# Optimization experiments

Measured on AMD Instinct MI355X. Metric: run time of the kernel, lower is better.

Reference implementation:

```python
import jax, jax.numpy as jnp
import numpy as np


def _vieta_pell_basis(x, degree):
    # Iterative recurrence: V0 = 2, V1 = x, Vn = x*V_{n-1} + V_{n-2}
    basis = [2.0 * jnp.ones_like(x), x]
    for _ in range(2, degree + 1):
        basis.append(x * basis[-1] + basis[-2])
    return jnp.stack(basis[: degree + 1], axis=-1)  # [b, i, d+1]


def setup_inputs() -> dict:
    key = jax.random.key(0)
    k1, k2 = jax.random.split(key)
    batch, input_dim, output_dim, degree = 4096, 1024, 1024, 8
    x = jax.random.normal(k1, (batch, input_dim), dtype=jnp.float32)
    std = 1.0 / (input_dim * (degree + 1))
    vp_coeffs = jax.random.normal(k2, (input_dim, output_dim, degree + 1), dtype=jnp.float32) * std
    return {"x": x, "vp_coeffs": vp_coeffs}


def reference(x, vp_coeffs):
    degree = vp_coeffs.shape[-1] - 1
    xt = jnp.tanh(x)  # [b, i]
    vp_basis = _vieta_pell_basis(xt, degree)  # [b, i, d+1]
    y = jnp.einsum("bid,iod->bo", vp_basis, vp_coeffs)
    return y
```

## Files before the change

kernel.cpp:

```cpp
#include <hip/hip_runtime.h>
#include <hip/hip_bf16.h>

typedef unsigned short u16;
typedef unsigned int   u32;
typedef unsigned long long u64;

#define BATCH 4096
#define IDIM  1024
#define ODIM  1024
#define NDEG  9
#define KTOT  (IDIM * NDEG)

#define BM 128
#define BN 128
#define BKK 64

typedef __attribute__((ext_vector_type(8))) short short8_t;
typedef __attribute__((ext_vector_type(4))) float f32x4;

__device__ __forceinline__ u16 f2bf(float f) {
    union { float f; u32 u; } v; v.f = f;
    u32 r = v.u + 0x7FFFu + ((v.u >> 16) & 1u);
    return (u16)(r >> 16);
}
__device__ __forceinline__ u32 pack2bf(float lo, float hi) {
    return (u32)f2bf(lo) | ((u32)f2bf(hi) << 16);
}

__device__ __forceinline__ void gl_lds16(const u16* g, u16* l) {
    __builtin_amdgcn_global_load_lds(
        (const __attribute__((address_space(1))) void*)g,
        (__attribute__((address_space(3))) void*)l,
        16, 0, 0);
}

#define PB_TI 128
#define PB_TO 8
#define PB_J  (PB_TO * NDEG)
#define PB_LS 132

#define NB_B   1024
#define NB_A   8192
#define NB_Z   256

__global__ void prep_kernel(const float* __restrict__ x,
                            const float* __restrict__ c,
                            u16* __restrict__ A, u16* __restrict__ Bt,
                            float* __restrict__ out) {
    __shared__ u16 lds[PB_J * PB_LS];
    const int bb  = blockIdx.x;
    const int tid = threadIdx.x;

    if (bb < NB_B) {
        const int i0 = (bb & 7) * PB_TI;
        const int o0 = (bb >> 3) * PB_TO;
        const float* src = c + (size_t)i0 * (ODIM * NDEG) + (size_t)o0 * NDEG;
#pragma unroll
        for (int t = 0; t < 36; ++t) {
            int f  = t * 256 + tid;
            int ii = f / PB_J;
            int j  = f - ii * PB_J;
            float v = src[(size_t)ii * (ODIM * NDEG) + j];
            lds[j * PB_LS + ii] = f2bf(v);
        }
        __syncthreads();
#pragma unroll
        for (int t = 0; t < 9; ++t) {
            int g   = t * 256 + tid;
            int j   = g >> 5;
            int ii4 = (g & 31) << 2;
            int o   = j / NDEG;
            int d   = j - o * NDEG;
            u64 v = *(const u64*)(lds + j * PB_LS + ii4);
            *(u64*)(Bt + (size_t)(o0 + o) * KTOT + d * 1024 + i0 + ii4) = v;
        }
    } else if (bb < NB_B + NB_A) {
        int t  = (bb - NB_B) * 256 + tid;
        int b  = t >> 9;
        int i2 = (t & 511) << 1;
        float2 xv = ((const float2*)x)[t];
        float t0 = tanhf(xv.x), t1 = tanhf(xv.y);
        u32* dst = (u32*)(A + (size_t)b * KTOT + i2);
        float a0 = 2.0f, a1 = 2.0f;
        float b0 = t0,  b1 = t1;
        dst[0]   = pack2bf(2.0f, 2.0f);
        dst[512] = pack2bf(t0, t1);
#pragma unroll
        for (int d = 2; d < NDEG; ++d) {
            float n0 = t0 * b0 + a0;
            float n1 = t1 * b1 + a1;
            dst[(size_t)d * 512] = pack2bf(n0, n1);
            a0 = b0; b0 = n0; a1 = b1; b1 = n1;
        }
    } else {
        int t = (bb - NB_B - NB_A) * 256 + tid;
        f32x4 z = (f32x4){0.f, 0.f, 0.f, 0.f};
#pragma unroll
        for (int r = 0; r < 16; ++r)
            ((f32x4*)out)[(size_t)r * (NB_Z * 256) + t] = z;
    }
}

__global__ __launch_bounds__(256, 2)
void gemm_kernel(const u16* __restrict__ A, const u16* __restrict__ B,
                 float* __restrict__ C, int kLen) {
    __shared__ __align__(16) u16 ldsA[BM * BKK];
    __shared__ __align__(16) u16 ldsB[BN * BKK];

    const int tid  = threadIdx.x;
    const int lane = tid & 63;
    const int wave = tid >> 6;
    const int quad = lane >> 4;
    const int l15  = lane & 15;
    const int wm   = wave & 1;
    const int wn   = wave >> 1;
    const int bm   = blockIdx.y;
    const int bn   = blockIdx.x;
    const int kStart = blockIdx.z * kLen;

    const u16* ga[4]; const u16* gb[4];
    u16* la[4]; u16* lb[4];
#pragma unroll
    for (int t = 0; t < 4; ++t) {
        int s  = t * 256 + tid;
        int r  = s >> 3;
        int sc = (s & 7) ^ (r & 7);
        ga[t] = A + (size_t)(bm * BM + r) * KTOT + kStart + sc * 8;
        gb[t] = B + (size_t)(bn * BN + r) * KTOT + kStart + sc * 8;
        la[t] = ldsA + s * 8;
        lb[t] = ldsB + s * 8;
    }

    f32x4 acc[4][4];
#pragma unroll
    for (int mt = 0; mt < 4; ++mt)
#pragma unroll
        for (int nt = 0; nt < 4; ++nt)
            acc[mt][nt] = (f32x4){0.f, 0.f, 0.f, 0.f};

    const int nIter = kLen / BKK;
    for (int it = 0; it < nIter; ++it) {
#pragma unroll
        for (int t = 0; t < 4; ++t) gl_lds16(ga[t], la[t]);
#pragma unroll
        for (int t = 0; t < 4; ++t) gl_lds16(gb[t], lb[t]);
        __syncthreads();

#pragma unroll
        for (int kk = 0; kk < 2; ++kk) {
            short8_t af[4], bfg[4];
#pragma unroll
            for (int mt = 0; mt < 4; ++mt) {
                int row = wm * 64 + mt * 16 + l15;
                int pc  = (kk * 4 + quad) ^ (row & 7);
                af[mt] = *(const short8_t*)(ldsA + (row * 8 + pc) * 8);
            }
#pragma unroll
            for (int nt = 0; nt < 4; ++nt) {
                int row = wn * 64 + nt * 16 + l15;
                int pc  = (kk * 4 + quad) ^ (row & 7);
                bfg[nt] = *(const short8_t*)(ldsB + (row * 8 + pc) * 8);
            }
#pragma unroll
            for (int mt = 0; mt < 4; ++mt)
#pragma unroll
                for (int nt = 0; nt < 4; ++nt)
                    acc[mt][nt] = __builtin_amdgcn_mfma_f32_16x16x32_bf16(
                        af[mt], bfg[nt], acc[mt][nt], 0, 0, 0);
        }
        __syncthreads();

#pragma unroll
        for (int t = 0; t < 4; ++t) { ga[t] += BKK; gb[t] += BKK; }
    }

#pragma unroll
    for (int mt = 0; mt < 4; ++mt) {
#pragma unroll
        for (int nt = 0; nt < 4; ++nt) {
            int row0 = bm * BM + wm * 64 + mt * 16 + quad * 4;
            int col  = bn * BN + wn * 64 + nt * 16 + l15;
#pragma unroll
            for (int r = 0; r < 4; ++r)
                atomicAdd(&C[(size_t)(row0 + r) * ODIM + col], acc[mt][nt][r]);
        }
    }
}

extern "C" void kernel_launch(void* const* d_in, const int* in_sizes, int n_in,
                              void* d_out, int out_size, void* d_ws, size_t ws_size,
                              hipStream_t stream) {
    const float* x      = (const float*)d_in[0];
    const float* coeffs = (const float*)d_in[1];
    float* out = (float*)d_out;

    u16* A  = (u16*)d_ws;
    u16* Bt = A + (size_t)BATCH * KTOT;

    prep_kernel<<<NB_B + NB_A + NB_Z, 256, 0, stream>>>(x, coeffs, A, Bt, out);

    dim3 grid(ODIM / BN, BATCH / BM, 2);
    gemm_kernel<<<grid, 256, 0, stream>>>(A, Bt, out, KTOT / 2);
}
```

Before: 216.4 us.

## Replace atomic split-K with partial buffers, reduce kernel, and XCD-aware block mapping

Split-K halves now store their results into two separate fp32 partial buffers in workspace, and a new reduce kernel sums them. This removes the output zeroing and the atomicAdd epilogue. The GEMM grid is flattened and remapped so each XCD gets a contiguous group of M tiles from one K half, to improve L2 locality for the shared A/B tiles. In exchange it adds an extra kernel launch plus about 48MB of extra global traffic for writing and reading the partials.

```diff
diff --git a/kernel.cpp b/kernel.cpp
--- a/kernel.cpp
+++ b/kernel.cpp
@@ -41,12 +41,10 @@
 
 #define NB_B   1024
 #define NB_A   8192
-#define NB_Z   256
 
 __global__ void prep_kernel(const float* __restrict__ x,
                             const float* __restrict__ c,
-                            u16* __restrict__ A, u16* __restrict__ Bt,
-                            float* __restrict__ out) {
+                            u16* __restrict__ A, u16* __restrict__ Bt) {
     __shared__ u16 lds[PB_J * PB_LS];
     const int bb  = blockIdx.x;
     const int tid = threadIdx.x;
@@ -74,7 +72,7 @@
             u64 v = *(const u64*)(lds + j * PB_LS + ii4);
             *(u64*)(Bt + (size_t)(o0 + o) * KTOT + d * 1024 + i0 + ii4) = v;
         }
-    } else if (bb < NB_B + NB_A) {
+    } else {
         int t  = (bb - NB_B) * 256 + tid;
         int b  = t >> 9;
         int i2 = (t & 511) << 1;
@@ -92,18 +90,12 @@
             dst[(size_t)d * 512] = pack2bf(n0, n1);
             a0 = b0; b0 = n0; a1 = b1; b1 = n1;
         }
-    } else {
-        int t = (bb - NB_B - NB_A) * 256 + tid;
-        f32x4 z = (f32x4){0.f, 0.f, 0.f, 0.f};
-#pragma unroll
-        for (int r = 0; r < 16; ++r)
-            ((f32x4*)out)[(size_t)r * (NB_Z * 256) + t] = z;
     }
 }
 
 __global__ __launch_bounds__(256, 2)
 void gemm_kernel(const u16* __restrict__ A, const u16* __restrict__ B,
-                 float* __restrict__ C, int kLen) {
+                 float* __restrict__ P) {
     __shared__ __align__(16) u16 ldsA[BM * BKK];
     __shared__ __align__(16) u16 ldsB[BN * BKK];
 
@@ -114,9 +106,15 @@
     const int l15  = lane & 15;
     const int wm   = wave & 1;
     const int wn   = wave >> 1;
-    const int bm   = blockIdx.y;
-    const int bn   = blockIdx.x;
-    const int kStart = blockIdx.z * kLen;
+
+    const int bid = blockIdx.x;
+    const int xcd = bid & 7;
+    const int loc = bid >> 3;
+    const int z   = xcd >> 2;
+    const int bm  = ((xcd & 3) << 3) | (loc >> 3);
+    const int bn  = loc & 7;
+    const int kStart = z * (KTOT / 2);
+    float* C = P + (size_t)z * BATCH * ODIM;
 
     const u16* ga[4]; const u16* gb[4];
     u16* la[4]; u16* lb[4];
@@ -138,7 +136,7 @@
         for (int nt = 0; nt < 4; ++nt)
             acc[mt][nt] = (f32x4){0.f, 0.f, 0.f, 0.f};
 
-    const int nIter = kLen / BKK;
+    const int nIter = (KTOT / 2) / BKK;
     for (int it = 0; it < nIter; ++it) {
 #pragma unroll
         for (int t = 0; t < 4; ++t) gl_lds16(ga[t], la[t]);
@@ -182,9 +180,16 @@
             int col  = bn * BN + wn * 64 + nt * 16 + l15;
 #pragma unroll
             for (int r = 0; r < 4; ++r)
-                atomicAdd(&C[(size_t)(row0 + r) * ODIM + col], acc[mt][nt][r]);
-        }
-    }
+                C[(size_t)(row0 + r) * ODIM + col] = acc[mt][nt][r];
+        }
+    }
+}
+
+__global__ void reduce_kernel(const float* __restrict__ P, float* __restrict__ out) {
+    int t = blockIdx.x * 256 + threadIdx.x;
+    f32x4 a = ((const f32x4*)P)[t];
+    f32x4 b = ((const f32x4*)(P + (size_t)BATCH * ODIM))[t];
+    ((f32x4*)out)[t] = a + b;
 }
 
 extern "C" void kernel_launch(void* const* d_in, const int* in_sizes, int n_in,
@@ -196,9 +201,9 @@
 
     u16* A  = (u16*)d_ws;
     u16* Bt = A + (size_t)BATCH * KTOT;
-
-    prep_kernel<<<NB_B + NB_A + NB_Z, 256, 0, stream>>>(x, coeffs, A, Bt, out);
-
-    dim3 grid(ODIM / BN, BATCH / BM, 2);
-    gemm_kernel<<<grid, 256, 0, stream>>>(A, Bt, out, KTOT / 2);
-}
+    float* P = (float*)(Bt + (size_t)ODIM * KTOT);
+
+    prep_kernel<<<NB_B + NB_A, 256, 0, stream>>>(x, coeffs, A, Bt);
+    gemm_kernel<<<512, 256, 0, stream>>>(A, Bt, P);
+    reduce_kernel<<<BATCH * ODIM / 1024, 256, 0, stream>>>(P, out);
+}
```

Result: faster. 187.3 us (-13.4%).
